# Kernel tuning notes

Hardware: AMD Instinct MI355X
Metric: run time of the kernel (lower is better)

The kernel has to match this reference:

```python
import jax, jax.numpy as jnp
import numpy as np

SEQ_LEN = 1
INPUT = 2048
HIDDEN = 2048
CLASSES = 10
K = int(np.floor(np.sqrt(HIDDEN)))            # avgKernelSize = 45
NUM_EH = (HIDDEN - K) // K + 1                # 45 pooled features
LENGTHS = (32, 128, 512)                      # EHlengths (window sizes)
EST_DIM = NUM_EH * len(LENGTHS) * 2           # mean + variance per (feature, window)
B = 8192


def setup_inputs() -> dict:
    key = jax.random.key(0)
    ks = jax.random.split(key, 7)
    s = 1.0 / np.sqrt(HIDDEN)
    u = lambda k, shape: jax.random.uniform(k, shape, jnp.float32, -s, s)
    return {
        "x": jax.random.normal(ks[0], (B, SEQ_LEN, INPUT), jnp.float32),
        "W_ih": u(ks[1], (HIDDEN, INPUT)),
        "W_hh": u(ks[2], (HIDDEN, HIDDEN)),
        "b_ih": u(ks[3], (HIDDEN,)),
        "b_hh": u(ks[4], (HIDDEN,)),
        "W_lin": u(ks[5], (CLASSES, HIDDEN + EST_DIM)),
        "b_lin": u(ks[6], (CLASSES,)),
    }


def _sliding_stats(pooled):
    """Causal sliding-window mean/variance over the batch/stream axis.

    pooled: (B, F). Returns (B, F, J, 2) with [..., 0]=mean, [..., 1]=var.
    This is the exact quantity the VarEH exponential histograms approximate
    (streaming mean/variance over the last L elements added).
    """
    n = pooled.shape[0]
    cs = jnp.cumsum(pooled, axis=0)
    cs2 = jnp.cumsum(pooled * pooled, axis=0)
    idx = jnp.arange(n)
    outs = []
    for L in LENGTHS:  # small fixed set of window lengths
        zpad = jnp.zeros((L,) + pooled.shape[1:], pooled.dtype)
        cs_l = jnp.concatenate([zpad, cs], axis=0)[:n]
        cs2_l = jnp.concatenate([zpad, cs2], axis=0)[:n]
        cnt = jnp.minimum(idx + 1, L).astype(pooled.dtype)[:, None]
        m = (cs - cs_l) / cnt
        v = (cs2 - cs2_l) / cnt - m * m
        outs.append(jnp.stack([m, v], axis=-1))  # (B, F, 2)
    return jnp.stack(outs, axis=2)  # (B, F, J, 2)


def reference(x, W_ih, W_hh, b_ih, b_hh, W_lin, b_lin):
    b = x.shape[0]
    # Elman RNN, batch_first, h0 = 0. Precompute input projection for all steps.
    xw = jnp.einsum("bsi,hi->bsh", x, W_ih) + b_ih + b_hh  # (B, S, H)

    def step(h, xt):
        h = jnp.tanh(xt + h @ W_hh.T)
        return h, h

    h0 = jnp.zeros((b, HIDDEN), x.dtype)
    _, hs = jax.lax.scan(step, h0, jnp.swapaxes(xw, 0, 1))  # (S, B, H)
    rnn_out = hs[-1]  # (B, H); with seq_len=1 this equals squeeze(rnn_out)

    # AvgPool1d(kernel=K, stride=K) over hidden dim -> (B, NUM_EH)
    pooled = rnn_out[:, : NUM_EH * K].reshape(b, NUM_EH, K).mean(axis=-1)

    # Streaming mean/var estimates across the batch stream (VarEH semantics)
    est = _sliding_stats(pooled).reshape(b, EST_DIM)

    lin_in = jnp.concatenate([rnn_out, est], axis=1)  # (B, H + EST_DIM)
    logits = lin_in @ W_lin.T + b_lin
    return jax.nn.softmax(logits, axis=1)
```

## Files before the change

kernel.cpp:

```cpp
#include <hip/hip_runtime.h>
#include <hip/hip_bf16.h>
#include <math.h>

typedef short s16x8 __attribute__((ext_vector_type(8)));
typedef float f32x4 __attribute__((ext_vector_type(4)));

__device__ inline unsigned short f2bf(float x) {
    unsigned int u = __float_as_uint(x);
    unsigned int r = (u + 0x7fffu + ((u >> 16) & 1u)) >> 16;
    return (unsigned short)r;
}
__device__ inline float bf2f(unsigned short u) {
    return __uint_as_float(((unsigned int)u) << 16);
}

__device__ inline float fast_tanh(float x) {
    float e = __expf(2.0f * x);
    return 1.0f - 2.0f * __builtin_amdgcn_rcpf(e + 1.0f);
}

__global__ void cvtprep_kernel(const float* __restrict__ W_ih,
                               const float* __restrict__ W_lin,
                               unsigned short* __restrict__ wb,
                               unsigned short* __restrict__ wlb,
                               float* __restrict__ zbase) {
    int blk = blockIdx.x;
    int tid = threadIdx.x;
    if (blk < 4096) {
        int i = blk * 256 + tid;
        float4 v = ((const float4*)W_ih)[i];
        ushort4 o; o.x = f2bf(v.x); o.y = f2bf(v.y); o.z = f2bf(v.z); o.w = f2bf(v.w);
        ((ushort4*)wb)[i] = o;
    } else if (blk < 4242) {
        int idx = (blk - 4096) * 256 + tid;
        if (idx < 37376) {
            int c = idx / 2336, k = idx - c * 2336;
            float v = (c < 10 && k < 2318) ? W_lin[c * 2318 + k] : 0.f;
            wlb[idx] = f2bf(v);
        }
    } else {
        int i = (blk - 4242) * 256 + tid;
        ((float4*)zbase)[i] = float4{0.f, 0.f, 0.f, 0.f};
    }
}


#define MFMA_(a, b, c) __builtin_amdgcn_mfma_f32_16x16x32_bf16(a, b, c, 0, 0, 0)

__device__ inline s16x8 frag_ld(const unsigned short* hbase, int row, int ksub, int quad) {
    int slot = (ksub * 4 + quad) ^ (row & 7);
    return *(const s16x8*)(hbase + row * 64 + slot * 8);
}

__device__ inline void stage_u(const unsigned short* __restrict__ gmat, int half,
                               int rowoff, int kt, unsigned short* lmat, int tid) {
    int r = tid >> 3, s = tid & 7;
    int lr = rowoff + r;
    int ks = (s ^ (lr & 7)) << 3;
    const unsigned short* gp = gmat + (size_t)(half * 128 + lr) * 2048 + kt * 64 + ks;
    __builtin_amdgcn_global_load_lds(
        (const __attribute__((address_space(1))) void*)gp,
        (__attribute__((address_space(3))) void*)(lmat + half * 8192 + lr * 64 + s * 8),
        16, 0, 0);
}

#define ISSUE_A(kt)                                                          \
    {                                                                        \
        const float* g0 = Xg + (size_t)(      ar) * 2048 + (kt) * 64 + as * 8; \
        const float* g1 = Xg + (size_t)(128 + ar) * 2048 + (kt) * 64 + as * 8; \
        ra0 = *(const float4*)g0; ra1 = *(const float4*)(g0 + 4);            \
        ra2 = *(const float4*)g1; ra3 = *(const float4*)(g1 + 4);            \
        asm volatile("" ::: "memory");                                       \
        const float* g2 = Xg + (size_t)( 64 + ar) * 2048 + (kt) * 64 + as * 8; \
        const float* g3 = Xg + (size_t)(192 + ar) * 2048 + (kt) * 64 + as * 8; \
        ra4 = *(const float4*)g2; ra5 = *(const float4*)(g2 + 4);            \
        ra6 = *(const float4*)g3; ra7 = *(const float4*)(g3 + 4);            \
    }

#define CVT8(v, lo, hi)                                                      \
    v[0] = f2bf(lo.x); v[1] = f2bf(lo.y); v[2] = f2bf(lo.z); v[3] = f2bf(lo.w); \
    v[4] = f2bf(hi.x); v[5] = f2bf(hi.y); v[6] = f2bf(hi.z); v[7] = f2bf(hi.w);

#define CVT_WRITE_TOP(dstA)                                                  \
    {                                                                        \
        s16x8 v0, v1;                                                        \
        CVT8(v0, ra0, ra1); CVT8(v1, ra2, ra3);                              \
        int off = ar * 64 + aslot * 8;                                       \
        *(s16x8*)((dstA) + off) = v0;                                        \
        *(s16x8*)((dstA) + 8192 + off) = v1;                                 \
    }
#define CVT_WRITE_BOT(dstA)                                                  \
    {                                                                        \
        s16x8 v0, v1;                                                        \
        CVT8(v0, ra4, ra5); CVT8(v1, ra6, ra7);                              \
        int off = (64 + ar) * 64 + aslot * 8;                                \
        *(s16x8*)((dstA) + off) = v0;                                        \
        *(s16x8*)((dstA) + 8192 + off) = v1;                                 \
    }

#define LOAD_B(ks)                                                       \
    b0 = frag_ld(Bh, bco +  0 + mrow, (ks), quad);                       \
    b1 = frag_ld(Bh, bco + 16 + mrow, (ks), quad);                       \
    b2 = frag_ld(Bh, bco + 32 + mrow, (ks), quad);                       \
    b3 = frag_ld(Bh, bco + 48 + mrow, (ks), quad);

#define LOAD_A(h, ks)                                                    \
    af0 = frag_ld(Ah, (h) * 64 +  0 + mrow, (ks), quad);                 \
    af1 = frag_ld(Ah, (h) * 64 + 16 + mrow, (ks), quad);                 \
    af2 = frag_ld(Ah, (h) * 64 + 32 + mrow, (ks), quad);                 \
    af3 = frag_ld(Ah, (h) * 64 + 48 + mrow, (ks), quad);

#define MFMA_H(hh)                                                       \
    acc[(hh)*4 + 0][0] = MFMA_(af0, b0, acc[(hh)*4 + 0][0]);             \
    acc[(hh)*4 + 0][1] = MFMA_(af0, b1, acc[(hh)*4 + 0][1]);             \
    acc[(hh)*4 + 0][2] = MFMA_(af0, b2, acc[(hh)*4 + 0][2]);             \
    acc[(hh)*4 + 0][3] = MFMA_(af0, b3, acc[(hh)*4 + 0][3]);             \
    acc[(hh)*4 + 1][0] = MFMA_(af1, b0, acc[(hh)*4 + 1][0]);             \
    acc[(hh)*4 + 1][1] = MFMA_(af1, b1, acc[(hh)*4 + 1][1]);             \
    acc[(hh)*4 + 1][2] = MFMA_(af1, b2, acc[(hh)*4 + 1][2]);             \
    acc[(hh)*4 + 1][3] = MFMA_(af1, b3, acc[(hh)*4 + 1][3]);             \
    acc[(hh)*4 + 2][0] = MFMA_(af2, b0, acc[(hh)*4 + 2][0]);             \
    acc[(hh)*4 + 2][1] = MFMA_(af2, b1, acc[(hh)*4 + 2][1]);             \
    acc[(hh)*4 + 2][2] = MFMA_(af2, b2, acc[(hh)*4 + 2][2]);             \
    acc[(hh)*4 + 2][3] = MFMA_(af2, b3, acc[(hh)*4 + 2][3]);             \
    acc[(hh)*4 + 3][0] = MFMA_(af3, b0, acc[(hh)*4 + 3][0]);             \
    acc[(hh)*4 + 3][1] = MFMA_(af3, b1, acc[(hh)*4 + 3][1]);             \
    acc[(hh)*4 + 3][2] = MFMA_(af3, b2, acc[(hh)*4 + 3][2]);             \
    acc[(hh)*4 + 3][3] = MFMA_(af3, b3, acc[(hh)*4 + 3][3]);

#define PHASE_CORE(hh)                                                   \
    __builtin_amdgcn_s_barrier();                                        \
    asm volatile("s_waitcnt lgkmcnt(0)" ::: "memory");                   \
    __builtin_amdgcn_s_setprio(1);                                       \
    MFMA_H(hh);                                                          \
    __builtin_amdgcn_s_setprio(0);

__global__ __launch_bounds__(512) void gemm_tanh_kernel(
    const float* __restrict__ X, const unsigned short* __restrict__ Bm,
    const float* __restrict__ b_ih, const float* __restrict__ b_hh,
    const unsigned short* __restrict__ Wl,
    float* __restrict__ pooled_t, float* __restrict__ linp)
{
    __shared__ __align__(16) unsigned short lds[2][2][16384];

    const int tid  = threadIdx.x;
    const int lane = tid & 63;
    const int wave = tid >> 6;
    const int wgid = blockIdx.x;
    const int xcd  = wgid & 7;
    const int idx  = wgid >> 3;
    const int rblk = xcd * 4 + (idx & 3);
    const int cblk = idx >> 2;
    const int row0 = rblk * 256;
    const int col0 = cblk * 256;
    const int wm   = wave >> 2;
    const int wn   = wave & 3;
    const int quad = lane >> 4;
    const int mrow = lane & 15;
    const int NT   = 32;

    const float* Xg = X + (size_t)row0 * 2048;
    const unsigned short* Bg = Bm + (size_t)col0 * 2048;

    const int ar = tid >> 3;
    const int as = tid & 7;
    const int aslot = as ^ (ar & 7);
    float4 ra0, ra1, ra2, ra3, ra4, ra5, ra6, ra7;

    f32x4 acc[8][4];
#pragma unroll
    for (int i = 0; i < 8; ++i)
#pragma unroll
        for (int j = 0; j < 4; ++j) acc[i][j] = f32x4{0.f, 0.f, 0.f, 0.f};

    ISSUE_A(0);
    stage_u(Bg, 0, 0,  0, lds[0][1], tid);  stage_u(Bg, 0, 64, 0, lds[0][1], tid);
    stage_u(Bg, 1, 0,  0, lds[0][1], tid);  stage_u(Bg, 1, 64, 0, lds[0][1], tid);
    asm volatile("s_waitcnt vmcnt(4)" ::: "memory");
    CVT_WRITE_TOP(lds[0][0]);
    CVT_WRITE_BOT(lds[0][0]);
    ISSUE_A(1);
    stage_u(Bg, 0, 0,  1, lds[1][1], tid);  stage_u(Bg, 0, 64, 1, lds[1][1], tid);
    asm volatile("s_waitcnt vmcnt(10)" ::: "memory");
    asm volatile("s_waitcnt lgkmcnt(0)" ::: "memory");
    __builtin_amdgcn_s_barrier();

    for (int t = 0; t < NT; ++t) {
        const int buf = t & 1;
        unsigned short* LA  = lds[buf][0];
        unsigned short* LB  = lds[buf][1];
        unsigned short* NLA = lds[buf ^ 1][0];
        unsigned short* NLB = lds[buf ^ 1][1];
        const unsigned short* Ah = LA + wm * 8192;
        const unsigned short* Bh = LB + (wn >> 1) * 8192;
        const int bco = (wn & 1) * 64;

        s16x8 b0, b1, b2, b3;
        s16x8 af0, af1, af2, af3;

        LOAD_B(0);
        LOAD_A(0, 0);
        if (t + 1 < NT) {
            stage_u(Bg, 1, 0,  t + 1, NLB, tid);
            stage_u(Bg, 1, 64, t + 1, NLB, tid);
        }
        asm volatile("s_waitcnt lgkmcnt(4)" ::: "memory");
        PHASE_CORE(0);
        __builtin_amdgcn_s_barrier();

        LOAD_A(1, 0);
        if (t + 1 < NT) {
            asm volatile("s_waitcnt vmcnt(8)" ::: "memory");
            CVT_WRITE_TOP(NLA);
        }
        PHASE_CORE(1);
        __builtin_amdgcn_s_barrier();

        LOAD_B(1);
        LOAD_A(0, 1);
        if (t + 1 < NT) {
            asm volatile("s_waitcnt vmcnt(4)" ::: "memory");
            CVT_WRITE_BOT(NLA);
        }
        if (t + 2 < NT) {
            ISSUE_A(t + 2);
        }
        asm volatile("s_waitcnt lgkmcnt(2)" ::: "memory");
        PHASE_CORE(0);
        __builtin_amdgcn_s_barrier();

        LOAD_A(1, 1);
        if (t + 2 < NT) {
            stage_u(Bg, 0, 0,  t + 2, LB, tid);
            stage_u(Bg, 0, 64, t + 2, LB, tid);
        }
        PHASE_CORE(1);
        if (t + 2 < NT) {
            asm volatile("s_waitcnt vmcnt(10)" ::: "memory");
        } else if (t + 1 < NT) {
            asm volatile("s_waitcnt vmcnt(0)" ::: "memory");
        }
        __builtin_amdgcn_s_barrier();
    }

    __syncthreads();
    unsigned short* T = &lds[0][0][0];
    float bias[4];
#pragma unroll
    for (int j = 0; j < 4; ++j) {
        int gc = col0 + wn * 64 + j * 16 + mrow;
        bias[j] = b_ih[gc] + b_hh[gc];
    }
#pragma unroll
    for (int i = 0; i < 8; ++i) {
#pragma unroll
        for (int rr = 0; rr < 4; ++rr) {
            int lrow = wm * 128 + i * 16 + quad * 4 + rr;
#pragma unroll
            for (int j = 0; j < 4; ++j) {
                int lcol = wn * 64 + j * 16 + mrow;
                float v = acc[i][j][rr] + bias[j];
                int cb = (lcol >> 3) ^ (lrow & 7);
                T[lrow * 256 + cb * 8 + (lcol & 7)] = f2bf(fast_tanh(v));
            }
        }
    }
    __syncthreads();

    int f0 = col0 / 45;
    for (int o = tid; o < 1792; o += 512) {
        int lrow = o / 7;
        int fi = o - lrow * 7;
        int f = f0 + fi;
        if (f < 45) {
            int wsb = f * 45, web = wsb + 45;
            int s = (wsb > col0) ? wsb : col0;
            int e = (web < col0 + 256) ? web : (col0 + 256);
            if (s < e) {
                float sum = 0.f;
                for (int c = s - col0; c < e - col0; ++c) {
                    int cb = (c >> 3) ^ (lrow & 7);
                    sum += bf2f(T[lrow * 256 + cb * 8 + (c & 7)]);
                }
                atomicAdd(&pooled_t[f * 8192 + row0 + lrow], sum);
            }
        }
    }

    f32x4 la = f32x4{0.f, 0.f, 0.f, 0.f};
    f32x4 lb = f32x4{0.f, 0.f, 0.f, 0.f};
    const int lr0 = wave * 32 + mrow;
    const int lr1 = lr0 + 16;
#pragma unroll
    for (int ks = 0; ks < 8; ++ks) {
        int c = ks * 32 + quad * 8;
        s16x8 bfrag = *(const s16x8*)(Wl + (size_t)mrow * 2336 + col0 + c);
        int cb0 = (c >> 3) ^ (lr0 & 7);
        s16x8 a0 = *(const s16x8*)(T + lr0 * 256 + cb0 * 8);
        la = MFMA_(a0, bfrag, la);
        int cb1 = (c >> 3) ^ (lr1 & 7);
        s16x8 a1 = *(const s16x8*)(T + lr1 * 256 + cb1 * 8);
        lb = MFMA_(a1, bfrag, lb);
    }
    if (mrow < 10) {
#pragma unroll
        for (int rr = 0; rr < 4; ++rr) {
            atomicAdd(&linp[(size_t)(row0 + wave * 32 + quad * 4 + rr) * 10 + mrow], la[rr]);
            atomicAdd(&linp[(size_t)(row0 + wave * 32 + 16 + quad * 4 + rr) * 10 + mrow], lb[rr]);
        }
    }
}

__global__ __launch_bounds__(256) void scan_kernel(
    const float* __restrict__ pooled_t,
    float* __restrict__ cs_t, float* __restrict__ cs2_t,
    float* __restrict__ sums1, float* __restrict__ sums2) {
    __shared__ float t1[256], t2[256];
    int f  = blockIdx.x >> 3;
    int ch = blockIdx.x & 7;
    int tid = threadIdx.x;
    const float S = 1.0f / 45.0f;
    const float* p = pooled_t + f * 8192 + ch * 1024;
    float4 v = ((const float4*)p)[tid];
    v.x *= S; v.y *= S; v.z *= S; v.w *= S;
    float q1[4], q2[4];
    q1[0] = v.x;          q2[0] = v.x * v.x;
    q1[1] = q1[0] + v.y;  q2[1] = q2[0] + v.y * v.y;
    q1[2] = q1[1] + v.z;  q2[2] = q2[1] + v.z * v.z;
    q1[3] = q1[2] + v.w;  q2[3] = q2[2] + v.w * v.w;
    float s1 = q1[3], s2 = q2[3];
    t1[tid] = s1; t2[tid] = s2;
    __syncthreads();
    for (int d = 1; d < 256; d <<= 1) {
        float a1 = (tid >= d) ? t1[tid - d] : 0.f;
        float a2 = (tid >= d) ? t2[tid - d] : 0.f;
        __syncthreads();
        t1[tid] += a1; t2[tid] += a2;
        __syncthreads();
    }
    float r1 = t1[tid] - s1, r2 = t2[tid] - s2;
    float4 o1, o2;
    o1.x = r1 + q1[0]; o1.y = r1 + q1[1]; o1.z = r1 + q1[2]; o1.w = r1 + q1[3];
    o2.x = r2 + q2[0]; o2.y = r2 + q2[1]; o2.z = r2 + q2[2]; o2.w = r2 + q2[3];
    ((float4*)(cs_t  + f * 8192 + ch * 1024))[tid] = o1;
    ((float4*)(cs2_t + f * 8192 + ch * 1024))[tid] = o2;
    if (tid == 255) {
        sums1[f * 8 + ch] = t1[255];
        sums2[f * 8 + ch] = t2[255];
    }
}

#define ESTRIDE 290
__global__ __launch_bounds__(128) void final_kernel(
    const float* __restrict__ cs_t, const float* __restrict__ cs2_t,
    const float* __restrict__ sums1, const float* __restrict__ sums2,
    const unsigned short* __restrict__ Wb, const float* __restrict__ linp,
    const float* __restrict__ b_lin, float* __restrict__ out) {
    __shared__ unsigned short Es[32 * ESTRIDE];
    __shared__ float eb1[45 * 8], eb2[45 * 8];
    __shared__ float comb[2][16][17];
    int tid = threadIdx.x;
    int lane = tid & 63;
    int wave = tid >> 6;
    int b0 = blockIdx.x * 32;

    if (tid < 45) {
        float a = 0.f, b = 0.f;
#pragma unroll
        for (int c = 0; c < 8; ++c) {
            eb1[tid * 8 + c] = a; a += sums1[tid * 8 + c];
            eb2[tid * 8 + c] = b; b += sums2[tid * 8 + c];
        }
    }
    __syncthreads();

    for (int i = tid; i < 135 * 32; i += 128) {
        int fj = i >> 5, r = i & 31;
        int f = fj / 3, j = fj - 3 * f;
        int b = b0 + r;
        int L = (j == 0) ? 32 : (j == 1) ? 128 : 512;
        const float* c1 = cs_t + f * 8192;
        const float* c2 = cs2_t + f * 8192;
        float a1 = c1[b] + eb1[f * 8 + (b >> 10)];
        float a2 = c2[b] + eb2[f * 8 + (b >> 10)];
        float p1 = 0.f, p2 = 0.f;
        if (b >= L) {
            int ix = b - L;
            p1 = c1[ix] + eb1[f * 8 + (ix >> 10)];
            p2 = c2[ix] + eb2[f * 8 + (ix >> 10)];
        }
        float cnt = (float)((b + 1 < L) ? (b + 1) : L);
        float m = (a1 - p1) / cnt;
        float v = (a2 - p2) / cnt - m * m;
        int d0 = f * 6 + j * 2;
        Es[r * ESTRIDE + d0]     = f2bf(m);
        Es[r * ESTRIDE + d0 + 1] = f2bf(v);
    }
    for (int i = tid; i < 32 * 18; i += 128) {
        int r = i / 18, d = 270 + i % 18;
        Es[r * ESTRIDE + d] = 0;
    }
    __syncthreads();

    const int quad = lane >> 4;
    const int mrow = lane & 15;

    f32x4 acc = f32x4{0.f, 0.f, 0.f, 0.f};
    const unsigned short* erow = Es + (wave * 16 + mrow) * ESTRIDE + quad * 8;
    const unsigned short* wrow = Wb + (size_t)mrow * 2336 + 2048 + quad * 8;
#pragma unroll
    for (int k = 0; k < 288; k += 32) {
        s16x8 a = *(const s16x8*)(erow + k);
        s16x8 b = *(const s16x8*)(wrow + k);
        acc = __builtin_amdgcn_mfma_f32_16x16x32_bf16(a, b, acc, 0, 0, 0);
    }
#pragma unroll
    for (int r = 0; r < 4; ++r) comb[wave][quad * 4 + r][mrow] = acc[r];
    __syncthreads();

    if (tid < 32) {
        int w = tid >> 4, r = tid & 15;
        int grow = b0 + w * 16 + r;
        float lg[10];
        float mx = -1e30f;
#pragma unroll
        for (int c = 0; c < 10; ++c) {
            lg[c] = comb[w][r][c] + linp[(size_t)grow * 10 + c] + b_lin[c];
            mx = fmaxf(mx, lg[c]);
        }
        float s = 0.f;
#pragma unroll
        for (int c = 0; c < 10; ++c) { lg[c] = expf(lg[c] - mx); s += lg[c]; }
        float inv = 1.0f / s;
#pragma unroll
        for (int c = 0; c < 10; ++c) out[(size_t)grow * 10 + c] = lg[c] * inv;
    }
}

extern "C" void kernel_launch(void* const* d_in, const int* in_sizes, int n_in,
                              void* d_out, int out_size, void* d_ws, size_t ws_size,
                              hipStream_t stream) {
    const float* x     = (const float*)d_in[0];
    const float* W_ih  = (const float*)d_in[1];
    const float* b_ih  = (const float*)d_in[3];
    const float* b_hh  = (const float*)d_in[4];
    const float* W_lin = (const float*)d_in[5];
    const float* b_lin = (const float*)d_in[6];
    float* out = (float*)d_out;

    char* ws = (char*)d_ws;
    unsigned short* wb  = (unsigned short*)(ws);
    float* pooled_t     = (float*)(ws + 8388608);
    float* linp         = (float*)(ws + 9863168);
    float* cs_t         = (float*)(ws + 10190848);
    float* cs2_t        = (float*)(ws + 11665408);
    unsigned short* wlb = (unsigned short*)(ws + 13139968);
    float* sums1        = (float*)(ws + 13214720);
    float* sums2        = (float*)(ws + 13216160);

    cvtprep_kernel<<<4682, 256, 0, stream>>>(W_ih, W_lin, wb, wlb, pooled_t);
    gemm_tanh_kernel<<<256, 512, 0, stream>>>(x, wb, b_ih, b_hh, wlb, pooled_t, linp);
    scan_kernel<<<360, 256, 0, stream>>>(pooled_t, cs_t, cs2_t, sums1, sums2);
    final_kernel<<<256, 128, 0, stream>>>(cs_t, cs2_t, sums1, sums2, wlb, linp, b_lin, out);
}
```

Baseline: 232.3 us.

## Double-buffer A-tile register staging to issue loads a full tile earlier

Adds a second set of float4 registers for the fp32 A tile and unrolls the k-loop by two so the two sets alternate. Global loads for tile t+2 are now issued at the start of iteration t instead of mid-iteration, which gives them more time to land before the bf16 convert and LDS write. The vmcnt and lgkmcnt waits are re-tuned to match. In exchange, each thread holds 16 more float4 registers (64 VGPRs), which may cause spills or lower occupancy at 512 threads per block.

```diff
diff --git a/kernel.cpp b/kernel.cpp
--- a/kernel.cpp
+++ b/kernel.cpp
@@ -64,35 +64,34 @@
         16, 0, 0);
 }
 
-#define ISSUE_A(kt)                                                          \
-    {                                                                        \
+#define ISSUE_AS(kt, S)                                                        \
+    {                                                                          \
         const float* g0 = Xg + (size_t)(      ar) * 2048 + (kt) * 64 + as * 8; \
         const float* g1 = Xg + (size_t)(128 + ar) * 2048 + (kt) * 64 + as * 8; \
-        ra0 = *(const float4*)g0; ra1 = *(const float4*)(g0 + 4);            \
-        ra2 = *(const float4*)g1; ra3 = *(const float4*)(g1 + 4);            \
-        asm volatile("" ::: "memory");                                       \
         const float* g2 = Xg + (size_t)( 64 + ar) * 2048 + (kt) * 64 + as * 8; \
         const float* g3 = Xg + (size_t)(192 + ar) * 2048 + (kt) * 64 + as * 8; \
-        ra4 = *(const float4*)g2; ra5 = *(const float4*)(g2 + 4);            \
-        ra6 = *(const float4*)g3; ra7 = *(const float4*)(g3 + 4);            \
-    }
-
-#define CVT8(v, lo, hi)                                                      \
-    v[0] = f2bf(lo.x); v[1] = f2bf(lo.y); v[2] = f2bf(lo.z); v[3] = f2bf(lo.w); \
+        S##0 = *(const float4*)g0; S##1 = *(const float4*)(g0 + 4);            \
+        S##2 = *(const float4*)g1; S##3 = *(const float4*)(g1 + 4);            \
+        S##4 = *(const float4*)g2; S##5 = *(const float4*)(g2 + 4);            \
+        S##6 = *(const float4*)g3; S##7 = *(const float4*)(g3 + 4);            \
+    }
+
+#define CVT8(v, lo, hi)                                                          \
+    v[0] = f2bf(lo.x); v[1] = f2bf(lo.y); v[2] = f2bf(lo.z); v[3] = f2bf(lo.w);  \
     v[4] = f2bf(hi.x); v[5] = f2bf(hi.y); v[6] = f2bf(hi.z); v[7] = f2bf(hi.w);
 
-#define CVT_WRITE_TOP(dstA)                                                  \
+#define CVT_WRITE_TOP(S, dstA)                                               \
     {                                                                        \
         s16x8 v0, v1;                                                        \
-        CVT8(v0, ra0, ra1); CVT8(v1, ra2, ra3);                              \
+        CVT8(v0, S##0, S##1); CVT8(v1, S##2, S##3);                          \
         int off = ar * 64 + aslot * 8;                                       \
         *(s16x8*)((dstA) + off) = v0;                                        \
         *(s16x8*)((dstA) + 8192 + off) = v1;                                 \
     }
-#define CVT_WRITE_BOT(dstA)                                                  \
+#define CVT_WRITE_BOT(S, dstA)                                               \
     {                                                                        \
         s16x8 v0, v1;                                                        \
-        CVT8(v0, ra4, ra5); CVT8(v1, ra6, ra7);                              \
+        CVT8(v0, S##4, S##5); CVT8(v1, S##6, S##7);                          \
         int off = (64 + ar) * 64 + aslot * 8;                                \
         *(s16x8*)((dstA) + off) = v0;                                        \
         *(s16x8*)((dstA) + 8192 + off) = v1;                                 \
@@ -128,12 +127,73 @@
     acc[(hh)*4 + 3][2] = MFMA_(af3, b2, acc[(hh)*4 + 3][2]);             \
     acc[(hh)*4 + 3][3] = MFMA_(af3, b3, acc[(hh)*4 + 3][3]);
 
-#define PHASE_CORE(hh)                                                   \
+#define PHASE_CORE_L(hh, lg)                                             \
     __builtin_amdgcn_s_barrier();                                        \
-    asm volatile("s_waitcnt lgkmcnt(0)" ::: "memory");                   \
+    asm volatile("s_waitcnt lgkmcnt(" lg ")" ::: "memory");              \
     __builtin_amdgcn_s_setprio(1);                                       \
     MFMA_H(hh);                                                          \
     __builtin_amdgcn_s_setprio(0);
+
+#define TILE_BODY(t, SI, SC)                                                 \
+    {                                                                        \
+        const int buf = (t) & 1;                                             \
+        unsigned short* LA  = lds[buf][0];                                   \
+        unsigned short* LB  = lds[buf][1];                                   \
+        unsigned short* NLA = lds[buf ^ 1][0];                               \
+        unsigned short* NLB = lds[buf ^ 1][1];                               \
+        const unsigned short* Ah = LA + wm * 8192;                           \
+        const unsigned short* Bh = LB + (wn >> 1) * 8192;                    \
+        const int bco = (wn & 1) * 64;                                       \
+        s16x8 b0, b1, b2, b3;                                                \
+        s16x8 af0, af1, af2, af3;                                            \
+              \
+        LOAD_B(0);                                                           \
+        LOAD_A(0, 0);                                                        \
+        if ((t) + 1 < NT) {                                                  \
+            stage_u(Bg, 1, 0,  (t) + 1, NLB, tid);                           \
+            stage_u(Bg, 1, 64, (t) + 1, NLB, tid);                           \
+        }                                                                    \
+        if ((t) + 2 < NT) { ISSUE_AS((t) + 2, SI); }                         \
+        PHASE_CORE_L(0, "0");                                                \
+        __builtin_amdgcn_s_barrier();                                        \
+                        \
+        LOAD_A(1, 0);                                                        \
+        if ((t) + 2 < NT) {                                                  \
+            asm volatile("s_waitcnt vmcnt(12)" ::: "memory");                \
+            CVT_WRITE_TOP(SC, NLA);                                          \
+            PHASE_CORE_L(1, "2");                                            \
+        } else if ((t) + 1 < NT) {                                           \
+            asm volatile("s_waitcnt vmcnt(4)" ::: "memory");                 \
+            CVT_WRITE_TOP(SC, NLA);                                          \
+            PHASE_CORE_L(1, "2");                                            \
+        } else {                                                             \
+            PHASE_CORE_L(1, "0");                                            \
+        }                                                                    \
+        __builtin_amdgcn_s_barrier();                                        \
+             \
+        LOAD_B(1);                                                           \
+        LOAD_A(0, 1);                                                        \
+        if ((t) + 1 < NT) {                                                  \
+            CVT_WRITE_BOT(SC, NLA);                                          \
+            PHASE_CORE_L(0, "2");                                            \
+        } else {                                                             \
+            PHASE_CORE_L(0, "0");                                            \
+        }                                                                    \
+        __builtin_amdgcn_s_barrier();                                        \
+                          \
+        LOAD_A(1, 1);                                                        \
+        if ((t) + 2 < NT) {                                                  \
+            stage_u(Bg, 0, 0,  (t) + 2, LB, tid);                            \
+            stage_u(Bg, 0, 64, (t) + 2, LB, tid);                            \
+        }                                                                    \
+        PHASE_CORE_L(1, "0");                                                \
+        if ((t) + 2 < NT) {                                                  \
+            asm volatile("s_waitcnt vmcnt(10)" ::: "memory");                \
+        } else if ((t) + 1 < NT) {                                           \
+            asm volatile("s_waitcnt vmcnt(0)" ::: "memory");                 \
+        }                                                                    \
+        __builtin_amdgcn_s_barrier();                                        \
+    }
 
 __global__ __launch_bounds__(512) void gemm_tanh_kernel(
     const float* __restrict__ X, const unsigned short* __restrict__ Bm,
@@ -165,7 +225,8 @@
     const int ar = tid >> 3;
     const int as = tid & 7;
     const int aslot = as ^ (ar & 7);
-    float4 ra0, ra1, ra2, ra3, ra4, ra5, ra6, ra7;
+    float4 A0_0, A0_1, A0_2, A0_3, A0_4, A0_5, A0_6, A0_7;
+    float4 A1_0, A1_1, A1_2, A1_3, A1_4, A1_5, A1_6, A1_7;
 
     f32x4 acc[8][4];
 #pragma unroll
@@ -173,74 +234,21 @@
 #pragma unroll
         for (int j = 0; j < 4; ++j) acc[i][j] = f32x4{0.f, 0.f, 0.f, 0.f};
 
-    ISSUE_A(0);
+    ISSUE_AS(0, A0_);
     stage_u(Bg, 0, 0,  0, lds[0][1], tid);  stage_u(Bg, 0, 64, 0, lds[0][1], tid);
     stage_u(Bg, 1, 0,  0, lds[0][1], tid);  stage_u(Bg, 1, 64, 0, lds[0][1], tid);
     asm volatile("s_waitcnt vmcnt(4)" ::: "memory");
-    CVT_WRITE_TOP(lds[0][0]);
-    CVT_WRITE_BOT(lds[0][0]);
-    ISSUE_A(1);
+    CVT_WRITE_TOP(A0_, lds[0][0]);
+    CVT_WRITE_BOT(A0_, lds[0][0]);
+    ISSUE_AS(1, A1_);
     stage_u(Bg, 0, 0,  1, lds[1][1], tid);  stage_u(Bg, 0, 64, 1, lds[1][1], tid);
     asm volatile("s_waitcnt vmcnt(10)" ::: "memory");
     asm volatile("s_waitcnt lgkmcnt(0)" ::: "memory");
     __builtin_amdgcn_s_barrier();
 
-    for (int t = 0; t < NT; ++t) {
-        const int buf = t & 1;
-        unsigned short* LA  = lds[buf][0];
-        unsigned short* LB  = lds[buf][1];
-        unsigned short* NLA = lds[buf ^ 1][0];
-        unsigned short* NLB = lds[buf ^ 1][1];
-        const unsigned short* Ah = LA + wm * 8192;
-        const unsigned short* Bh = LB + (wn >> 1) * 8192;
-        const int bco = (wn & 1) * 64;
-
-        s16x8 b0, b1, b2, b3;
-        s16x8 af0, af1, af2, af3;
-
-        LOAD_B(0);
-        LOAD_A(0, 0);
-        if (t + 1 < NT) {
-            stage_u(Bg, 1, 0,  t + 1, NLB, tid);
-            stage_u(Bg, 1, 64, t + 1, NLB, tid);
-        }
-        asm volatile("s_waitcnt lgkmcnt(4)" ::: "memory");
-        PHASE_CORE(0);
-        __builtin_amdgcn_s_barrier();
-
-        LOAD_A(1, 0);
-        if (t + 1 < NT) {
-            asm volatile("s_waitcnt vmcnt(8)" ::: "memory");
-            CVT_WRITE_TOP(NLA);
-        }
-        PHASE_CORE(1);
-        __builtin_amdgcn_s_barrier();
-
-        LOAD_B(1);
-        LOAD_A(0, 1);
-        if (t + 1 < NT) {
-            asm volatile("s_waitcnt vmcnt(4)" ::: "memory");
-            CVT_WRITE_BOT(NLA);
-        }
-        if (t + 2 < NT) {
-            ISSUE_A(t + 2);
-        }
-        asm volatile("s_waitcnt lgkmcnt(2)" ::: "memory");
-        PHASE_CORE(0);
-        __builtin_amdgcn_s_barrier();
-
-        LOAD_A(1, 1);
-        if (t + 2 < NT) {
-            stage_u(Bg, 0, 0,  t + 2, LB, tid);
-            stage_u(Bg, 0, 64, t + 2, LB, tid);
-        }
-        PHASE_CORE(1);
-        if (t + 2 < NT) {
-            asm volatile("s_waitcnt vmcnt(10)" ::: "memory");
-        } else if (t + 1 < NT) {
-            asm volatile("s_waitcnt vmcnt(0)" ::: "memory");
-        }
-        __builtin_amdgcn_s_barrier();
+    for (int t = 0; t < NT; t += 2) {
+        TILE_BODY(t,     A0_, A1_);
+        TILE_BODY(t + 1, A1_, A0_);
     }
 
     __syncthreads();
```

Result: slower. 462.5 us (+99.1%).

## Stage fp32 X tiles through LDS bounce buffers via async global_load_lds

Applied to the files above, without the earlier changes.

Replaces the per-thread register prefetch of fp32 X tiles (eight float4 registers per thread) with asynchronous global_load_lds transfers into two fp32 LDS bounce buffers. The bf16 conversion is now split into four 64-row chunks read back from LDS and interleaved between the MFMA phases. The aim is to free VGPRs and let X loads overlap compute without register staging. In exchange it adds 32KB of LDS, extra LDS round trips, and more barriers and waitcnt points per k-step, which may reduce occupancy or stall the MFMA pipeline.

```diff
diff --git a/kernel.cpp b/kernel.cpp
--- a/kernel.cpp
+++ b/kernel.cpp
@@ -3,6 +3,7 @@
 #include <math.h>
 
 typedef short s16x8 __attribute__((ext_vector_type(8)));
+typedef short s16x4 __attribute__((ext_vector_type(4)));
 typedef float f32x4 __attribute__((ext_vector_type(4)));
 
 __device__ inline unsigned short f2bf(float x) {
@@ -64,38 +65,31 @@
         16, 0, 0);
 }
 
-#define ISSUE_A(kt)                                                          \
-    {                                                                        \
-        const float* g0 = Xg + (size_t)(      ar) * 2048 + (kt) * 64 + as * 8; \
-        const float* g1 = Xg + (size_t)(128 + ar) * 2048 + (kt) * 64 + as * 8; \
-        ra0 = *(const float4*)g0; ra1 = *(const float4*)(g0 + 4);            \
-        ra2 = *(const float4*)g1; ra3 = *(const float4*)(g1 + 4);            \
-        asm volatile("" ::: "memory");                                       \
-        const float* g2 = Xg + (size_t)( 64 + ar) * 2048 + (kt) * 64 + as * 8; \
-        const float* g3 = Xg + (size_t)(192 + ar) * 2048 + (kt) * 64 + as * 8; \
-        ra4 = *(const float4*)g2; ra5 = *(const float4*)(g2 + 4);            \
-        ra6 = *(const float4*)g3; ra7 = *(const float4*)(g3 + 4);            \
-    }
-
-#define CVT8(v, lo, hi)                                                      \
-    v[0] = f2bf(lo.x); v[1] = f2bf(lo.y); v[2] = f2bf(lo.z); v[3] = f2bf(lo.w); \
-    v[4] = f2bf(hi.x); v[5] = f2bf(hi.y); v[6] = f2bf(hi.z); v[7] = f2bf(hi.w);
-
-#define CVT_WRITE_TOP(dstA)                                                  \
-    {                                                                        \
-        s16x8 v0, v1;                                                        \
-        CVT8(v0, ra0, ra1); CVT8(v1, ra2, ra3);                              \
-        int off = ar * 64 + aslot * 8;                                       \
-        *(s16x8*)((dstA) + off) = v0;                                        \
-        *(s16x8*)((dstA) + 8192 + off) = v1;                                 \
-    }
-#define CVT_WRITE_BOT(dstA)                                                  \
-    {                                                                        \
-        s16x8 v0, v1;                                                        \
-        CVT8(v0, ra4, ra5); CVT8(v1, ra6, ra7);                              \
-        int off = (64 + ar) * 64 + aslot * 8;                                \
-        *(s16x8*)((dstA) + off) = v0;                                        \
-        *(s16x8*)((dstA) + 8192 + off) = v1;                                 \
+__device__ inline void stage_bx(const float* __restrict__ Xg, int j, int u, int kt,
+                                float* bptr, int tid) {
+    const float* gp = Xg + (size_t)(j * 64 + u * 32 + (tid >> 4)) * 2048
+                      + kt * 64 + (tid & 15) * 4;
+    __builtin_amdgcn_global_load_lds(
+        (const __attribute__((address_space(1))) void*)gp,
+        (__attribute__((address_space(3))) void*)(bptr + u * 2048 + tid * 4), 16, 0, 0);
+}
+
+#define CVT_CHUNK(j, b, dstA)                                                  \
+    {                                                                          \
+        const float* bb = bounce[b];                                           \
+        float4 f0 = *(const float4*)(bb + tid * 4);                            \
+        float4 f1 = *(const float4*)(bb + 2048 + tid * 4);                     \
+        unsigned short* bas = (dstA) + ((j) >> 1) * 8192 + ((j) & 1) * 4096;   \
+        int R0 = tid >> 4;                                                     \
+        int s4 = (tid & 15) >> 1;                                              \
+        int sb = (tid & 1) * 4;                                                \
+        s16x4 o0, o1;                                                          \
+        o0[0] = (short)f2bf(f0.x); o0[1] = (short)f2bf(f0.y);                  \
+        o0[2] = (short)f2bf(f0.z); o0[3] = (short)f2bf(f0.w);                  \
+        o1[0] = (short)f2bf(f1.x); o1[1] = (short)f2bf(f1.y);                  \
+        o1[2] = (short)f2bf(f1.z); o1[3] = (short)f2bf(f1.w);                  \
+        *(s16x4*)(bas + R0 * 64 + (s4 ^ (R0 & 7)) * 8 + sb) = o0;              \
+        *(s16x4*)(bas + (32 + R0) * 64 + (s4 ^ (R0 & 7)) * 8 + sb) = o1;       \
     }
 
 #define LOAD_B(ks)                                                       \
@@ -142,6 +136,7 @@
     float* __restrict__ pooled_t, float* __restrict__ linp)
 {
     __shared__ __align__(16) unsigned short lds[2][2][16384];
+    __shared__ __align__(16) float bounce[2][4096];
 
     const int tid  = threadIdx.x;
     const int lane = tid & 63;
@@ -162,27 +157,30 @@
     const float* Xg = X + (size_t)row0 * 2048;
     const unsigned short* Bg = Bm + (size_t)col0 * 2048;
 
-    const int ar = tid >> 3;
-    const int as = tid & 7;
-    const int aslot = as ^ (ar & 7);
-    float4 ra0, ra1, ra2, ra3, ra4, ra5, ra6, ra7;
-
     f32x4 acc[8][4];
 #pragma unroll
     for (int i = 0; i < 8; ++i)
 #pragma unroll
         for (int j = 0; j < 4; ++j) acc[i][j] = f32x4{0.f, 0.f, 0.f, 0.f};
 
-    ISSUE_A(0);
+    stage_bx(Xg, 0, 0, 0, bounce[0], tid);  stage_bx(Xg, 0, 1, 0, bounce[0], tid);
+    stage_bx(Xg, 2, 0, 0, bounce[1], tid);  stage_bx(Xg, 2, 1, 0, bounce[1], tid);
     stage_u(Bg, 0, 0,  0, lds[0][1], tid);  stage_u(Bg, 0, 64, 0, lds[0][1], tid);
     stage_u(Bg, 1, 0,  0, lds[0][1], tid);  stage_u(Bg, 1, 64, 0, lds[0][1], tid);
     asm volatile("s_waitcnt vmcnt(4)" ::: "memory");
-    CVT_WRITE_TOP(lds[0][0]);
-    CVT_WRITE_BOT(lds[0][0]);
-    ISSUE_A(1);
+    __builtin_amdgcn_s_barrier();
+    CVT_CHUNK(0, 0, lds[0][0]);
+    CVT_CHUNK(2, 1, lds[0][0]);
+    asm volatile("s_waitcnt lgkmcnt(0)" ::: "memory");
+    __builtin_amdgcn_s_barrier();
+    stage_bx(Xg, 1, 0, 0, bounce[0], tid);  stage_bx(Xg, 1, 1, 0, bounce[0], tid);
+    asm volatile("s_waitcnt vmcnt(0)" ::: "memory");
+    __builtin_amdgcn_s_barrier();
+    CVT_CHUNK(1, 0, lds[0][0]);
+    asm volatile("s_waitcnt lgkmcnt(0)" ::: "memory");
+    __builtin_amdgcn_s_barrier();
     stage_u(Bg, 0, 0,  1, lds[1][1], tid);  stage_u(Bg, 0, 64, 1, lds[1][1], tid);
-    asm volatile("s_waitcnt vmcnt(10)" ::: "memory");
-    asm volatile("s_waitcnt lgkmcnt(0)" ::: "memory");
+    stage_bx(Xg, 3, 0, 0, bounce[1], tid);  stage_bx(Xg, 3, 1, 0, bounce[1], tid);
     __builtin_amdgcn_s_barrier();
 
     for (int t = 0; t < NT; ++t) {
@@ -203,30 +201,44 @@
         if (t + 1 < NT) {
             stage_u(Bg, 1, 0,  t + 1, NLB, tid);
             stage_u(Bg, 1, 64, t + 1, NLB, tid);
+            stage_bx(Xg, 0, 0, t + 1, bounce[0], tid);
+            stage_bx(Xg, 0, 1, t + 1, bounce[0], tid);
+            asm volatile("s_waitcnt vmcnt(4)" ::: "memory");
+        } else {
+            asm volatile("s_waitcnt vmcnt(0)" ::: "memory");
         }
         asm volatile("s_waitcnt lgkmcnt(4)" ::: "memory");
         PHASE_CORE(0);
+        CVT_CHUNK(3, 1, LA);
+        asm volatile("s_waitcnt lgkmcnt(0)" ::: "memory");
         __builtin_amdgcn_s_barrier();
 
         LOAD_A(1, 0);
         if (t + 1 < NT) {
-            asm volatile("s_waitcnt vmcnt(8)" ::: "memory");
-            CVT_WRITE_TOP(NLA);
+            stage_bx(Xg, 2, 0, t + 1, bounce[1], tid);
+            stage_bx(Xg, 2, 1, t + 1, bounce[1], tid);
+            asm volatile("s_waitcnt vmcnt(2)" ::: "memory");
         }
         PHASE_CORE(1);
+        if (t + 1 < NT) {
+            CVT_CHUNK(0, 0, NLA);
+            asm volatile("s_waitcnt lgkmcnt(0)" ::: "memory");
+        }
         __builtin_amdgcn_s_barrier();
 
         LOAD_B(1);
         LOAD_A(0, 1);
         if (t + 1 < NT) {
-            asm volatile("s_waitcnt vmcnt(4)" ::: "memory");
-            CVT_WRITE_BOT(NLA);
-        }
-        if (t + 2 < NT) {
-            ISSUE_A(t + 2);
-        }
-        asm volatile("s_waitcnt lgkmcnt(2)" ::: "memory");
+            stage_bx(Xg, 1, 0, t + 1, bounce[0], tid);
+            stage_bx(Xg, 1, 1, t + 1, bounce[0], tid);
+            asm volatile("s_waitcnt vmcnt(2)" ::: "memory");
+        }
+        asm volatile("s_waitcnt lgkmcnt(4)" ::: "memory");
         PHASE_CORE(0);
+        if (t + 1 < NT) {
+            CVT_CHUNK(2, 1, NLA);
+            asm volatile("s_waitcnt lgkmcnt(0)" ::: "memory");
+        }
         __builtin_amdgcn_s_barrier();
 
         LOAD_A(1, 1);
@@ -234,11 +246,19 @@
             stage_u(Bg, 0, 0,  t + 2, LB, tid);
             stage_u(Bg, 0, 64, t + 2, LB, tid);
         }
+        if (t + 1 < NT) {
+            stage_bx(Xg, 3, 0, t + 1, bounce[1], tid);
+            stage_bx(Xg, 3, 1, t + 1, bounce[1], tid);
+        }
+        if (t + 2 < NT) {
+            asm volatile("s_waitcnt vmcnt(4)" ::: "memory");
+        } else if (t + 1 < NT) {
+            asm volatile("s_waitcnt vmcnt(2)" ::: "memory");
+        }
         PHASE_CORE(1);
-        if (t + 2 < NT) {
-            asm volatile("s_waitcnt vmcnt(10)" ::: "memory");
-        } else if (t + 1 < NT) {
-            asm volatile("s_waitcnt vmcnt(0)" ::: "memory");
+        if (t + 1 < NT) {
+            CVT_CHUNK(1, 0, NLA);
+            asm volatile("s_waitcnt lgkmcnt(0)" ::: "memory");
         }
         __builtin_amdgcn_s_barrier();
     }
@@ -267,11 +287,11 @@
     }
     __syncthreads();
 
-    int f0 = col0 / 45;
+    int f0p = col0 / 45;
     for (int o = tid; o < 1792; o += 512) {
         int lrow = o / 7;
         int fi = o - lrow * 7;
-        int f = f0 + fi;
+        int f = f0p + fi;
         if (f < 45) {
             int wsb = f * 45, web = wsb + 45;
             int s = (wsb > col0) ? wsb : col0;
```

After: 254.3 us. 9.5% more time.
